# Optimization experiments

Measured on AMD Instinct MI355X. Metric: run time of the kernel, lower is better.

## Reference

```python
import jax, jax.numpy as jnp
import numpy as np

B, S, D, H = 2, 2048, 2048, 16
HD = D // H  # head_dim = 128
ROPE_BASE = 10000.0


def _rope_interleaved(x, cos, sin):
    # x: [B, S, H, HD]; cos/sin: [S, HD//2]
    xe = x[..., 0::2]
    xo = x[..., 1::2]
    c = cos[None, :, None, :]
    s = sin[None, :, None, :]
    oe = xe * c - xo * s
    oo = xe * s + xo * c
    # re-interleave pairs back to last dim
    return jnp.stack([oe, oo], axis=-1).reshape(x.shape)


def setup_inputs() -> dict:
    key = jax.random.key(0)
    k0, k1, k2, k3 = jax.random.split(key, 4)
    scale = D ** -0.5
    x = jax.random.normal(k0, (B, S, D), dtype=jnp.float32)
    wqk = jax.random.normal(k1, (2 * D, D), dtype=jnp.float32) * scale
    wv = jax.random.normal(k2, (D, D), dtype=jnp.float32) * scale
    wo = jax.random.normal(k3, (D, D), dtype=jnp.float32) * scale
    return {"x": x, "wqk": wqk, "wv": wv, "wo": wo}


def reference(x, wqk, wv, wo):
    b, s, d = x.shape
    # fused QK projection -> [B, S, 2, H, HD]
    xqk = (x @ wqk.T).reshape(b, s, 2, H, HD)
    xq = xqk[:, :, 0]
    xk = xqk[:, :, 1]
    xv = (x @ wv.T).reshape(b, s, H, HD)

    # interleaved rotary embedding (seqlen_offset=0, no-cache path)
    inv_freq = 1.0 / (ROPE_BASE ** (jnp.arange(0, HD, 2, dtype=jnp.float32) / HD))
    freqs = jnp.arange(s, dtype=jnp.float32)[:, None] * inv_freq[None, :]  # [S, HD//2]
    cos, sin = jnp.cos(freqs), jnp.sin(freqs)
    xq = _rope_interleaved(xq, cos, sin)
    xk = _rope_interleaved(xk, cos, sin)

    # causal scaled-dot-product attention
    scores = jnp.einsum("bqhd,bkhd->bhqk", xq, xk) * (HD ** -0.5)
    causal = jnp.tril(jnp.ones((s, s), dtype=bool))
    scores = jnp.where(causal[None, None], scores, jnp.finfo(scores.dtype).min)
    probs = jax.nn.softmax(scores, axis=-1)
    out = jnp.einsum("bhqk,bkhd->bqhd", probs, xv).reshape(b, s, d)
    return out @ wo.T
```

## Files before the change

kernel.cpp:

```cpp
#include <hip/hip_runtime.h>
#include <hip/hip_bf16.h>

#define NB 2
#define SEQ 2048
#define DMODEL 2048
#define NH 16
#define HD 128
#define QSCALE (0.08838834764831845f * 1.44269504088896f)
#define THRL2 11.5f

using bf16x8 = __attribute__((ext_vector_type(8))) __bf16;
using f32x4  = __attribute__((ext_vector_type(4))) float;

#define MFMA16 __builtin_amdgcn_mfma_f32_16x16x32_bf16

typedef __attribute__((address_space(1))) const void* gptr_t;
typedef __attribute__((address_space(3))) void* lptr_t;

__device__ inline void gload_lds16(const unsigned short* g, unsigned short* l) {
    __builtin_amdgcn_global_load_lds((gptr_t)g, (lptr_t)l, 16, 0, 0);
}

__device__ inline unsigned short f2b(float f) {
    unsigned u = __builtin_bit_cast(unsigned, f);
    u += 0x7FFF + ((u >> 16) & 1);
    return (unsigned short)(u >> 16);
}
__device__ inline float b2f(unsigned short h) {
    return __builtin_bit_cast(float, (unsigned)h << 16);
}
__device__ inline float fexp2(float x) {
    float r;
    asm("v_exp_f32 %0, %1" : "=v"(r) : "v"(x));
    return r;
}
__device__ inline unsigned cvtpk(float a, float b) {
    unsigned r;
    asm("v_cvt_pk_bf16_f32 %0, %1, %2" : "=v"(r) : "v"(a), "v"(b));
    return r;
}

__global__ void cast_all(const float* __restrict__ x, const float* __restrict__ wqk,
                         const float* __restrict__ wv, const float* __restrict__ wo,
                         unsigned short* __restrict__ xb, unsigned short* __restrict__ wb,
                         float2* __restrict__ tab) {
    int idx = blockIdx.x * 256 + threadIdx.x;
    if (idx < 6291456) {
        const float* src; unsigned short* dst; int off;
        if (idx < 2097152)      { src = x;   dst = xb;             off = 0; }
        else if (idx < 4194304) { src = wqk; dst = wb;             off = 2097152; }
        else if (idx < 5242880) { src = wv;  dst = wb + 8388608;   off = 4194304; }
        else                    { src = wo;  dst = wb + 12582912;  off = 5242880; }
        int i = (idx - off) * 4;
        float4 v = *reinterpret_cast<const float4*>(src + i);
        ushort4 o;
        o.x = f2b(v.x); o.y = f2b(v.y); o.z = f2b(v.z); o.w = f2b(v.w);
        *reinterpret_cast<ushort4*>(dst + i) = o;
    } else {
        int k = idx - 6291456;
        int i = k & 63;
        int s = k >> 6;
        float inv = exp2f(-13.287712379549449f * (float)i * (1.0f / 64.0f));
        float ang = (float)s * inv;
        float sn, cs;
        sincosf(ang, &sn, &cs);
        tab[k] = make_float2(cs, sn);
    }
}

__global__ __launch_bounds__(512) void gemm256(const unsigned short* __restrict__ A,
                                               const unsigned short* __restrict__ Bw,
                                               unsigned short* __restrict__ qb,
                                               unsigned short* __restrict__ kbp,
                                               unsigned short* __restrict__ vt,
                                               const float2* __restrict__ tab,
                                               int M, int N, int K) {
    __shared__ __align__(16) char lds[131072];
    int tid = threadIdx.x;
    int lane = tid & 63;
    int wid = tid >> 6;
    int wm = wid >> 2, wn = wid & 3;
    int row0 = blockIdx.y * 256;
    int col0 = blockIdx.x * 256;
    int lr = lane & 15, g = lane >> 4;

    const unsigned short* srcA[4];
    const unsigned short* srcB[4];
#pragma unroll
    for (int i = 0; i < 4; i++) {
        int chunk = i * 512 + tid;
        int ksub = chunk >> 10;
        int cw = chunk & 1023;
        int row = cw >> 2, c = cw & 3;
        int cs = c ^ ((row >> 1) & 3);
        srcA[i] = A  + (size_t)(row0 + row) * K + ksub * 32 + cs * 8;
        srcB[i] = Bw + (size_t)(col0 + row) * K + ksub * 32 + cs * 8;
    }

    int offA[8][2], offB[4][2];
#pragma unroll
    for (int i = 0; i < 8; i++) {
        int row = wm * 128 + i * 16 + lr;
#pragma unroll
        for (int ks = 0; ks < 2; ks++)
            offA[i][ks] = ks * 16384 + row * 64 + ((g ^ ((row >> 1) & 3)) * 16);
    }
#pragma unroll
    for (int j = 0; j < 4; j++) {
        int row = wn * 64 + j * 16 + lr;
#pragma unroll
        for (int ks = 0; ks < 2; ks++)
            offB[j][ks] = 32768 + ks * 16384 + row * 64 + ((g ^ ((row >> 1) & 3)) * 16);
    }

    f32x4 acc[8][4] = {};
    int NT = K >> 6;

#define STAGE256(t) {                                                                 \
        int kb_ = (t) * 64;                                                           \
        int bs_ = ((t) & 1) * 65536;                                                  \
        _Pragma("unroll")                                                             \
        for (int i_ = 0; i_ < 4; i_++)                                                \
            gload_lds16(srcA[i_] + kb_,                                               \
                (unsigned short*)(lds + bs_ + (i_ * 512 + (tid & ~63)) * 16));        \
        _Pragma("unroll")                                                             \
        for (int i_ = 0; i_ < 4; i_++)                                                \
            gload_lds16(srcB[i_] + kb_,                                               \
                (unsigned short*)(lds + bs_ + 32768 + (i_ * 512 + (tid & ~63)) * 16)); \
    }

    STAGE256(0);
    for (int t = 0; t < NT; ++t) {
        if (t + 1 < NT) {
            STAGE256(t + 1);
            asm volatile("s_waitcnt vmcnt(8)" ::: "memory");
        } else {
            asm volatile("s_waitcnt vmcnt(0)" ::: "memory");
        }
        __builtin_amdgcn_s_barrier();
        __builtin_amdgcn_sched_barrier(0);

        const char* bufc = lds + (t & 1) * 65536;
        bf16x8 av[4], bv[4];

#pragma unroll
        for (int j = 0; j < 4; j++) bv[j] = *reinterpret_cast<const bf16x8*>(bufc + offB[j][0]);
#pragma unroll
        for (int i = 0; i < 4; i++) av[i] = *reinterpret_cast<const bf16x8*>(bufc + offA[i][0]);
        asm volatile("s_waitcnt lgkmcnt(0)" ::: "memory");
        __builtin_amdgcn_sched_barrier(0);
        __builtin_amdgcn_s_setprio(1);
#pragma unroll
        for (int i = 0; i < 4; i++)
#pragma unroll
            for (int j = 0; j < 4; j++)
                acc[i][j] = MFMA16(av[i], bv[j], acc[i][j], 0, 0, 0);
        __builtin_amdgcn_s_setprio(0);

#pragma unroll
        for (int i = 0; i < 4; i++) av[i] = *reinterpret_cast<const bf16x8*>(bufc + offA[4 + i][0]);
        asm volatile("s_waitcnt lgkmcnt(0)" ::: "memory");
        __builtin_amdgcn_sched_barrier(0);
        __builtin_amdgcn_s_setprio(1);
#pragma unroll
        for (int i = 0; i < 4; i++)
#pragma unroll
            for (int j = 0; j < 4; j++)
                acc[4 + i][j] = MFMA16(av[i], bv[j], acc[4 + i][j], 0, 0, 0);
        __builtin_amdgcn_s_setprio(0);

#pragma unroll
        for (int j = 0; j < 4; j++) bv[j] = *reinterpret_cast<const bf16x8*>(bufc + offB[j][1]);
#pragma unroll
        for (int i = 0; i < 4; i++) av[i] = *reinterpret_cast<const bf16x8*>(bufc + offA[i][1]);
        asm volatile("s_waitcnt lgkmcnt(0)" ::: "memory");
        __builtin_amdgcn_sched_barrier(0);
        __builtin_amdgcn_s_setprio(1);
#pragma unroll
        for (int i = 0; i < 4; i++)
#pragma unroll
            for (int j = 0; j < 4; j++)
                acc[i][j] = MFMA16(av[i], bv[j], acc[i][j], 0, 0, 0);
        __builtin_amdgcn_s_setprio(0);

#pragma unroll
        for (int i = 0; i < 4; i++) av[i] = *reinterpret_cast<const bf16x8*>(bufc + offA[4 + i][1]);
        asm volatile("s_waitcnt lgkmcnt(0)" ::: "memory");
        __builtin_amdgcn_sched_barrier(0);
        __builtin_amdgcn_s_barrier();
        __builtin_amdgcn_sched_barrier(0);
        __builtin_amdgcn_s_setprio(1);
#pragma unroll
        for (int i = 0; i < 4; i++)
#pragma unroll
            for (int j = 0; j < 4; j++)
                acc[4 + i][j] = MFMA16(av[i], bv[j], acc[4 + i][j], 0, 0, 0);
        __builtin_amdgcn_s_setprio(0);
    }
#undef STAGE256

    int orow = g * 4;
    int bx = blockIdx.x;
    if (bx < 16) {
        const bool isQ = (bx < 8);
        unsigned short* dst = isQ ? qb : kbp;
#pragma unroll
        for (int i = 0; i < 8; i++) {
#pragma unroll
            for (int j = 0; j < 4; j++) {
                int c = col0 + wn * 64 + j * 16 + lr;
                int cc = c & 2047;
                int h = cc >> 7, d = cc & 127, i2 = d >> 1;
                int odd = lr & 1;
#pragma unroll
                for (int r = 0; r < 4; r++) {
                    int trow = row0 + wm * 128 + i * 16 + orow + r;
                    int s = trow & (SEQ - 1), bb2 = trow >> 11;
                    float v = acc[i][j][r];
                    float pv = __shfl_xor(v, 1);
                    float2 cssn = tab[s * 64 + i2];
                    float out = odd ? (pv * cssn.y + v * cssn.x)
                                    : (v * cssn.x - pv * cssn.y);
                    if (isQ) out *= QSCALE;
                    dst[((size_t)((bb2 * NH + h) * SEQ + s)) * HD + d] = f2b(out);
                }
            }
        }
    } else {
#pragma unroll
        for (int i = 0; i < 8; i++) {
#pragma unroll
            for (int j = 0; j < 4; j++) {
                int cc = col0 + wn * 64 + j * 16 + lr - 4096;
                int h = cc >> 7, d = cc & 127;
                int trow0 = row0 + wm * 128 + i * 16 + orow;
                int s0 = trow0 & (SEQ - 1), bb2 = trow0 >> 11;
                int bh = bb2 * NH + h;
                ushort4 o4;
                o4.x = f2b(acc[i][j][0]);
                o4.y = f2b(acc[i][j][1]);
                o4.z = f2b(acc[i][j][2]);
                o4.w = f2b(acc[i][j][3]);
                *reinterpret_cast<ushort4*>(vt + ((size_t)bh * HD + d) * SEQ + s0) = o4;
            }
        }
    }
}

__global__ __launch_bounds__(512) void gemm8p(const unsigned short* __restrict__ A,
                                              const unsigned short* __restrict__ Bw,
                                              float* __restrict__ Cout,
                                              int M, int N, int K) {
    __shared__ __align__(16) char lds[98304];
    int tid = threadIdx.x;
    int lane = tid & 63;
    int wid = tid >> 6;
    int wm = wid >> 2, wn = wid & 3;
    int row0 = blockIdx.y * 128;
    int col0 = blockIdx.x * 256;
    int lr = lane & 15, g = lane >> 4;

    const unsigned short* srcA[2];
    const unsigned short* srcB[4];
#pragma unroll
    for (int i = 0; i < 2; i++) {
        int chunk = i * 512 + tid;
        int ksub = chunk >> 9;
        int cw = chunk & 511;
        int row = cw >> 2, c = cw & 3;
        int cs = c ^ ((row >> 1) & 3);
        srcA[i] = A + (size_t)(row0 + row) * K + ksub * 32 + cs * 8;
    }
#pragma unroll
    for (int i = 0; i < 4; i++) {
        int chunk = i * 512 + tid;
        int ksub = chunk >> 10;
        int cw = chunk & 1023;
        int row = cw >> 2, c = cw & 3;
        int cs = c ^ ((row >> 1) & 3);
        srcB[i] = Bw + (size_t)(col0 + row) * K + ksub * 32 + cs * 8;
    }

    int offA[4][2], offB[4][2];
#pragma unroll
    for (int i = 0; i < 4; i++) {
        int row = wm * 64 + i * 16 + lr;
#pragma unroll
        for (int ks = 0; ks < 2; ks++)
            offA[i][ks] = ks * 8192 + row * 64 + ((g ^ ((row >> 1) & 3)) * 16);
    }
#pragma unroll
    for (int j = 0; j < 4; j++) {
        int row = wn * 64 + j * 16 + lr;
#pragma unroll
        for (int ks = 0; ks < 2; ks++)
            offB[j][ks] = ks * 16384 + row * 64 + ((g ^ ((row >> 1) & 3)) * 16);
    }

    f32x4 acc[4][4] = {};
    int NT = K >> 6;

#define STAGE8(t) {                                                                   \
        int kb_ = (t) * 64;                                                           \
        int bs_ = ((t) & 1) * 49152;                                                  \
        _Pragma("unroll")                                                             \
        for (int i_ = 0; i_ < 2; i_++)                                                \
            gload_lds16(srcA[i_] + kb_,                                               \
                (unsigned short*)(lds + bs_ + (i_ * 512 + (tid & ~63)) * 16));        \
        _Pragma("unroll")                                                             \
        for (int i_ = 0; i_ < 4; i_++)                                                \
            gload_lds16(srcB[i_] + kb_,                                               \
                (unsigned short*)(lds + bs_ + 16384 + (i_ * 512 + (tid & ~63)) * 16)); \
    }

    STAGE8(0);
    for (int t = 0; t < NT; ++t) {
        if (t + 1 < NT) {
            STAGE8(t + 1);
            asm volatile("s_waitcnt vmcnt(6)" ::: "memory");
        } else {
            asm volatile("s_waitcnt vmcnt(0)" ::: "memory");
        }
        __builtin_amdgcn_s_barrier();
        __builtin_amdgcn_sched_barrier(0);

        const char* ab = lds + (t & 1) * 49152;
        const char* bb = ab + 16384;

        bf16x8 b[4][2], a[2][2];
#pragma unroll
        for (int j = 0; j < 4; j++)
#pragma unroll
            for (int ks = 0; ks < 2; ks++)
                b[j][ks] = *reinterpret_cast<const bf16x8*>(bb + offB[j][ks]);
#pragma unroll
        for (int i = 0; i < 2; i++)
#pragma unroll
            for (int ks = 0; ks < 2; ks++)
                a[i][ks] = *reinterpret_cast<const bf16x8*>(ab + offA[i][ks]);
        asm volatile("s_waitcnt lgkmcnt(0)" ::: "memory");
        __builtin_amdgcn_sched_barrier(0);
        __builtin_amdgcn_s_setprio(1);
#pragma unroll
        for (int ks = 0; ks < 2; ks++)
#pragma unroll
            for (int i = 0; i < 2; i++)
#pragma unroll
                for (int j = 0; j < 4; j++)
                    acc[i][j] = MFMA16(a[i][ks], b[j][ks], acc[i][j], 0, 0, 0);
        __builtin_amdgcn_s_setprio(0);

        bf16x8 a2[2][2];
#pragma unroll
        for (int i = 0; i < 2; i++)
#pragma unroll
            for (int ks = 0; ks < 2; ks++)
                a2[i][ks] = *reinterpret_cast<const bf16x8*>(ab + offA[2 + i][ks]);
        asm volatile("s_waitcnt lgkmcnt(0)" ::: "memory");
        __builtin_amdgcn_sched_barrier(0);
        __builtin_amdgcn_s_barrier();
        __builtin_amdgcn_sched_barrier(0);
        __builtin_amdgcn_s_setprio(1);
#pragma unroll
        for (int ks = 0; ks < 2; ks++)
#pragma unroll
            for (int i = 0; i < 2; i++)
#pragma unroll
                for (int j = 0; j < 4; j++)
                    acc[2 + i][j] = MFMA16(a2[i][ks], b[j][ks], acc[2 + i][j], 0, 0, 0);
        __builtin_amdgcn_s_setprio(0);
    }
#undef STAGE8

    int orow = g * 4;
#pragma unroll
    for (int i = 0; i < 4; i++) {
#pragma unroll
        for (int j = 0; j < 4; j++) {
            int r0 = row0 + wm * 64 + i * 16 + orow;
            int c  = col0 + wn * 64 + j * 16 + lr;
#pragma unroll
            for (int r = 0; r < 4; r++)
                Cout[(size_t)(r0 + r) * N + c] = acc[i][j][r];
        }
    }
}

__global__ __launch_bounds__(64, 2) void attn8(const unsigned short* __restrict__ Q,
                                               const unsigned short* __restrict__ Kb,
                                               const unsigned short* __restrict__ Vt,
                                               unsigned short* __restrict__ O) {
    __shared__ __align__(16) char lds[18432];

    int lane = threadIdx.x;
    int bid = blockIdx.x;
    int qt = 63 - (bid >> 5);
    int bh = bid & 31;
    int q0 = qt * 32;
    int ktiles = qt + 1;
    int lr = lane & 15;
    int g  = lane >> 4;
    int g4 = g * 4;
    int lk = g * 8;

    const unsigned short* Qp = Q  + (size_t)bh * SEQ * HD;
    const unsigned short* Kp = Kb + (size_t)bh * SEQ * HD;
    const unsigned short* Vp = Vt + (size_t)bh * HD * SEQ;
    char* pl = lds + 16384;
    int b = bh >> 4;
    int h = bh & 15;

    int srcoff[8];
#pragma unroll
    for (int i2 = 0; i2 < 8; ++i2) {
        int r = i2 * 4 + g;
        srcoff[i2] = r * HD + ((lr ^ (r & 7)) * 8);
    }

#define STAGEK32(bufbase, kvbase)                                                   \
    {                                                                               \
        const unsigned short* kbase = Kp + (size_t)(kvbase) * HD;                   \
        _Pragma("unroll")                                                           \
        for (int i2 = 0; i2 < 8; ++i2)                                              \
            gload_lds16(kbase + srcoff[i2],                                         \
                        (unsigned short*)(lds + (bufbase) + i2 * 1024));            \
    }

    bf16x8 qf[2][4];
#pragma unroll
    for (int f = 0; f < 2; f++)
#pragma unroll
        for (int kb = 0; kb < 4; kb++)
            qf[f][kb] = *reinterpret_cast<const bf16x8*>(Qp + (size_t)(q0 + f * 16 + lr) * HD + kb * 32 + lk);

    f32x4 oacc[2][8] = {};
    float m[2] = { -1e30f, -1e30f }, l[2] = { 0.0f, 0.0f };
    int qrow[2] = { q0 + lr, q0 + 16 + lr };

    STAGEK32(0, 0);

    int cur = 0;
    for (int t = 0; t < ktiles; ++t) {
        int kv0 = t * 32;
        if (t + 1 < ktiles) {
            STAGEK32((cur ^ 1) * 8192, kv0 + 32);
            asm volatile("s_waitcnt vmcnt(8)" ::: "memory");
        } else {
            asm volatile("s_waitcnt vmcnt(0)" ::: "memory");
        }
        __builtin_amdgcn_sched_barrier(0);

        char* kb_c = lds + cur * 8192;
        f32x4 s[2][2] = {};
#pragma unroll
        for (int kb = 0; kb < 4; kb++) {
#pragma unroll
            for (int jj = 0; jj < 2; jj++) {
                int row = jj * 16 + lr;
                int cin = ((kb * 4 + g) ^ (row & 7));
                bf16x8 kf = *reinterpret_cast<const bf16x8*>(kb_c + row * 256 + cin * 16);
                s[0][jj] = MFMA16(kf, qf[0][kb], s[0][jj], 0, 0, 0);
                s[1][jj] = MFMA16(kf, qf[1][kb], s[1][jj], 0, 0, 0);
            }
        }

        bf16x8 vf[8];
#pragma unroll
        for (int db = 0; db < 8; db++)
            vf[db] = *reinterpret_cast<const bf16x8*>(Vp + (size_t)(db * 16 + lr) * SEQ + kv0 + lk);

#pragma unroll
        for (int f = 0; f < 2; f++) {
            int q = qrow[f];
            bool full = (kv0 + 31 <= q0 + f * 16);
            float mx = -1e30f;
            if (full) {
#pragma unroll
                for (int jj = 0; jj < 2; jj++)
#pragma unroll
                    for (int r = 0; r < 4; r++)
                        mx = fmaxf(mx, s[f][jj][r]);
            } else {
#pragma unroll
                for (int jj = 0; jj < 2; jj++)
#pragma unroll
                    for (int r = 0; r < 4; r++) {
                        int kv = kv0 + jj * 16 + g4 + r;
                        float v = (kv <= q) ? s[f][jj][r] : -1e30f;
                        s[f][jj][r] = v;
                        mx = fmaxf(mx, v);
                    }
            }
            mx = fmaxf(mx, __shfl_xor(mx, 16));
            mx = fmaxf(mx, __shfl_xor(mx, 32));

            if (!__all(mx <= m[f] + THRL2)) {
                float mn = fmaxf(m[f], mx);
                float sc = fexp2(m[f] - mn);
                m[f] = mn;
                l[f] *= sc;
#pragma unroll
                for (int db = 0; db < 8; db++)
#pragma unroll
                    for (int r = 0; r < 4; r++)
                        oacc[f][db][r] *= sc;
            }

            int row = f * 16 + lr;
            int rb = row * 64;
            int sw = (row & 3) << 4;
            float rs = 0.0f;
#pragma unroll
            for (int jj = 0; jj < 2; jj++)
#pragma unroll
                for (int hh = 0; hh < 2; hh++) {
                    float p0 = fexp2(s[f][jj][2 * hh]     - m[f]);
                    float p1 = fexp2(s[f][jj][2 * hh + 1] - m[f]);
                    rs += p0 + p1;
                    unsigned pk = cvtpk(p0, p1);
                    int colb = jj * 32 + g * 8 + 4 * hh;
                    *reinterpret_cast<unsigned*>(pl + rb + (colb ^ sw)) = pk;
                }
            rs += __shfl_xor(rs, 16);
            rs += __shfl_xor(rs, 32);
            l[f] += rs;
        }

        asm volatile("s_waitcnt lgkmcnt(0)" ::: "memory");
        __builtin_amdgcn_sched_barrier(0);

        bf16x8 pb[2];
#pragma unroll
        for (int f = 0; f < 2; f++) {
            int row = f * 16 + lr;
            int off = row * 64 + ((g * 16) ^ ((row & 3) << 4));
            pb[f] = *reinterpret_cast<const bf16x8*>(pl + off);
        }
#pragma unroll
        for (int db = 0; db < 8; db++) {
            oacc[0][db] = MFMA16(vf[db], pb[0], oacc[0][db], 0, 0, 0);
            oacc[1][db] = MFMA16(vf[db], pb[1], oacc[1][db], 0, 0, 0);
        }

        cur ^= 1;
    }

#pragma unroll
    for (int f = 0; f < 2; f++) {
        float inv = 1.0f / l[f];
        int q = q0 + f * 16 + lr;
        unsigned short* op = O + ((size_t)(b * SEQ + q)) * DMODEL + h * HD;
#pragma unroll
        for (int db = 0; db < 8; db++) {
            ushort4 o4;
            o4.x = f2b(oacc[f][db][0] * inv);
            o4.y = f2b(oacc[f][db][1] * inv);
            o4.z = f2b(oacc[f][db][2] * inv);
            o4.w = f2b(oacc[f][db][3] * inv);
            *reinterpret_cast<ushort4*>(op + db * 16 + g4) = o4;
        }
    }
#undef STAGEK32
}

extern "C" void kernel_launch(void* const* d_in, const int* in_sizes, int n_in,
                              void* d_out, int out_size, void* d_ws, size_t ws_size,
                              hipStream_t stream) {
    const float* x   = (const float*)d_in[0];
    const float* wqk = (const float*)d_in[1];
    const float* wv  = (const float*)d_in[2];
    const float* wo  = (const float*)d_in[3];

    unsigned short* xb  = (unsigned short*)d_ws;
    unsigned short* wb  = xb  + (size_t)8388608;
    unsigned short* qb  = wb  + (size_t)16777216;
    unsigned short* kb  = qb  + (size_t)8388608;
    unsigned short* vt  = kb  + (size_t)8388608;
    unsigned short* ao  = vt  + (size_t)8388608;
    float2* tab = (float2*)(ao + (size_t)8388608);

    cast_all<<<25088, 256, 0, stream>>>(x, wqk, wv, wo, xb, wb, tab);

    gemm256<<<dim3(24, 16), 512, 0, stream>>>(xb, wb, qb, kb, vt, tab, 4096, 6144, 2048);

    attn8<<<2048, 64, 0, stream>>>(qb, kb, vt, ao);

    gemm8p<<<dim3(8, 32), 512, 0, stream>>>(ao, wb + 12582912, d_out ? (float*)d_out : nullptr, 4096, 2048, 2048);
}
```

Baseline: 291.0 us.

## Split GEMM tile staging into half-K chunks interleaved with MFMA phases

The QKV projection GEMM previously issued all global-to-LDS loads for the next K tile in one burst before computing. It now splits each 64-wide K tile into two 32-wide halves and issues them piecemeal between MFMA phases. The first half of tile t+2 goes into the current buffer once its first half has been consumed, guarded by a mid-iteration barrier. This spreads memory traffic across compute and deepens prefetch, at the cost of an extra barrier per iteration and more intricate vmcnt accounting.

```diff
diff --git a/kernel.cpp b/kernel.cpp
--- a/kernel.cpp
+++ b/kernel.cpp
@@ -84,17 +84,29 @@
     int col0 = blockIdx.x * 256;
     int lr = lane & 15, g = lane >> 4;
 
-    const unsigned short* srcA[4];
-    const unsigned short* srcB[4];
-#pragma unroll
-    for (int i = 0; i < 4; i++) {
+    const unsigned short *pA[2], *pB[2];
+    int ldsc[2];
+#pragma unroll
+    for (int i = 0; i < 2; i++) {
         int chunk = i * 512 + tid;
-        int ksub = chunk >> 10;
-        int cw = chunk & 1023;
-        int row = cw >> 2, c = cw & 3;
+        int row = chunk >> 2, c = chunk & 3;
         int cs = c ^ ((row >> 1) & 3);
-        srcA[i] = A  + (size_t)(row0 + row) * K + ksub * 32 + cs * 8;
-        srcB[i] = Bw + (size_t)(col0 + row) * K + ksub * 32 + cs * 8;
+        pA[i] = A  + (size_t)(row0 + row) * K + cs * 8;
+        pB[i] = Bw + (size_t)(col0 + row) * K + cs * 8;
+        ldsc[i] = (i * 512 + (tid & ~63)) * 16;
+    }
+
+#define STG_A(bs_, kb_, h) {                                                          \
+        _Pragma("unroll")                                                             \
+        for (int i_ = 0; i_ < 2; i_++)                                                \
+            gload_lds16(pA[i_] + (kb_) + (h) * 32,                                    \
+                (unsigned short*)(lds + (bs_) + (h) * 16384 + ldsc[i_]));             \
+    }
+#define STG_B(bs_, kb_, h) {                                                          \
+        _Pragma("unroll")                                                             \
+        for (int i_ = 0; i_ < 2; i_++)                                                \
+            gload_lds16(pB[i_] + (kb_) + (h) * 32,                                    \
+                (unsigned short*)(lds + (bs_) + 32768 + (h) * 16384 + ldsc[i_]));     \
     }
 
     int offA[8][2], offB[4][2];
@@ -116,37 +128,27 @@
     f32x4 acc[8][4] = {};
     int NT = K >> 6;
 
-#define STAGE256(t) {                                                                 \
-        int kb_ = (t) * 64;                                                           \
-        int bs_ = ((t) & 1) * 65536;                                                  \
-        _Pragma("unroll")                                                             \
-        for (int i_ = 0; i_ < 4; i_++)                                                \
-            gload_lds16(srcA[i_] + kb_,                                               \
-                (unsigned short*)(lds + bs_ + (i_ * 512 + (tid & ~63)) * 16));        \
-        _Pragma("unroll")                                                             \
-        for (int i_ = 0; i_ < 4; i_++)                                                \
-            gload_lds16(srcB[i_] + kb_,                                               \
-                (unsigned short*)(lds + bs_ + 32768 + (i_ * 512 + (tid & ~63)) * 16)); \
-    }
-
-    STAGE256(0);
+    STG_A(0, 0, 0); STG_B(0, 0, 0); STG_A(0, 0, 1); STG_B(0, 0, 1);
+    STG_A(65536, 64, 0); STG_B(65536, 64, 0);
+
     for (int t = 0; t < NT; ++t) {
-        if (t + 1 < NT) {
-            STAGE256(t + 1);
-            asm volatile("s_waitcnt vmcnt(8)" ::: "memory");
-        } else {
-            asm volatile("s_waitcnt vmcnt(0)" ::: "memory");
-        }
+        const char* bufc = lds + (t & 1) * 65536;
+        int bufn = ((t + 1) & 1) * 65536;
+        bool h1 = (t + 1 < NT);
+        bool h2 = (t + 2 < NT);
+
+        if (h1) asm volatile("s_waitcnt vmcnt(8)" ::: "memory");
+        else    asm volatile("s_waitcnt vmcnt(4)" ::: "memory");
         __builtin_amdgcn_s_barrier();
         __builtin_amdgcn_sched_barrier(0);
 
-        const char* bufc = lds + (t & 1) * 65536;
         bf16x8 av[4], bv[4];
 
 #pragma unroll
         for (int j = 0; j < 4; j++) bv[j] = *reinterpret_cast<const bf16x8*>(bufc + offB[j][0]);
 #pragma unroll
         for (int i = 0; i < 4; i++) av[i] = *reinterpret_cast<const bf16x8*>(bufc + offA[i][0]);
+        if (h1) STG_A(bufn, (t + 1) * 64, 1);
         asm volatile("s_waitcnt lgkmcnt(0)" ::: "memory");
         __builtin_amdgcn_sched_barrier(0);
         __builtin_amdgcn_s_setprio(1);
@@ -159,6 +161,7 @@
 
 #pragma unroll
         for (int i = 0; i < 4; i++) av[i] = *reinterpret_cast<const bf16x8*>(bufc + offA[4 + i][0]);
+        if (h1) STG_B(bufn, (t + 1) * 64, 1);
         asm volatile("s_waitcnt lgkmcnt(0)" ::: "memory");
         __builtin_amdgcn_sched_barrier(0);
         __builtin_amdgcn_s_setprio(1);
@@ -169,10 +172,16 @@
                 acc[4 + i][j] = MFMA16(av[i], bv[j], acc[4 + i][j], 0, 0, 0);
         __builtin_amdgcn_s_setprio(0);
 
+        if (h1) asm volatile("s_waitcnt vmcnt(8)" ::: "memory");
+        else    asm volatile("s_waitcnt vmcnt(0)" ::: "memory");
+        __builtin_amdgcn_s_barrier();
+        __builtin_amdgcn_sched_barrier(0);
+
 #pragma unroll
         for (int j = 0; j < 4; j++) bv[j] = *reinterpret_cast<const bf16x8*>(bufc + offB[j][1]);
 #pragma unroll
         for (int i = 0; i < 4; i++) av[i] = *reinterpret_cast<const bf16x8*>(bufc + offA[i][1]);
+        if (h2) STG_A((t & 1) * 65536, (t + 2) * 64, 0);
         asm volatile("s_waitcnt lgkmcnt(0)" ::: "memory");
         __builtin_amdgcn_sched_barrier(0);
         __builtin_amdgcn_s_setprio(1);
@@ -185,9 +194,8 @@
 
 #pragma unroll
         for (int i = 0; i < 4; i++) av[i] = *reinterpret_cast<const bf16x8*>(bufc + offA[4 + i][1]);
-        asm volatile("s_waitcnt lgkmcnt(0)" ::: "memory");
-        __builtin_amdgcn_sched_barrier(0);
-        __builtin_amdgcn_s_barrier();
+        if (h2) STG_B((t & 1) * 65536, (t + 2) * 64, 0);
+        asm volatile("s_waitcnt lgkmcnt(0)" ::: "memory");
         __builtin_amdgcn_sched_barrier(0);
         __builtin_amdgcn_s_setprio(1);
 #pragma unroll
@@ -197,7 +205,8 @@
                 acc[4 + i][j] = MFMA16(av[i], bv[j], acc[4 + i][j], 0, 0, 0);
         __builtin_amdgcn_s_setprio(0);
     }
-#undef STAGE256
+#undef STG_A
+#undef STG_B
 
     int orow = g * 4;
     int bx = blockIdx.x;
```

New measurement: 280.0 us. 1.04x faster.
